# Kernel tuning notes

Measured on AMD Instinct MI355X. Metric: run time of the kernel, lower is better.

Reference implementation:

```python
import jax, jax.numpy as jnp
import numpy as np

N_NODES = 50000
N_EDGES = 100000
N_PAIRS = 1600000
IN_DIM = 2816
MAP_HID = 512
IN_CH = 512
HID_CH = 256
OUT_CH = 128


def _dense(x, W, b):
    return x @ W + b


def setup_inputs() -> dict:
    key = jax.random.key(0)
    ks = jax.random.split(key, 20)
    m_emb = jax.random.normal(ks[0], (N_NODES, IN_DIM), dtype=jnp.float32)
    he_v_idx_pos = jax.random.randint(ks[1], (N_PAIRS,), 0, N_NODES)
    he_e_idx_pos = jnp.sort(jax.random.randint(ks[2], (N_PAIRS,), 0, N_EDGES))
    he_v_idx_neg = jax.random.randint(ks[3], (N_PAIRS,), 0, N_NODES)
    he_e_idx_neg = jnp.sort(jax.random.randint(ks[4], (N_PAIRS,), 0, N_EDGES))

    def lin(k, din, dout):
        k1, k2 = jax.random.split(k)
        s = 1.0 / np.sqrt(din)
        W = jax.random.uniform(k1, (din, dout), minval=-s, maxval=s, dtype=jnp.float32)
        b = jax.random.uniform(k2, (dout,), minval=-s, maxval=s, dtype=jnp.float32)
        return W, b

    W0, b0 = lin(ks[5], IN_DIM, MAP_HID)
    W1, b1 = lin(ks[6], MAP_HID, MAP_HID)
    W2, b2 = lin(ks[7], MAP_HID, IN_CH)
    Wt1, bt1 = lin(ks[8], IN_CH, HID_CH)   # HGNN layer 1 theta
    Wt2, bt2 = lin(ks[9], HID_CH, OUT_CH)  # HGNN layer 2 theta

    return dict(
        m_emb=m_emb,
        he_v_idx_pos=he_v_idx_pos, he_e_idx_pos=he_e_idx_pos,
        he_v_idx_neg=he_v_idx_neg, he_e_idx_neg=he_e_idx_neg,
        W0=W0, b0=b0, W1=W1, b1=b1, W2=W2, b2=b2,
        Wt1=Wt1, bt1=bt1, Wt2=Wt2, bt2=bt2,
    )


def _hg_mean_aggr(X, v_idx, e_idx, n_edges, n_nodes):
    # v2e: mean of member-vertex features per hyperedge
    e_sum = jax.ops.segment_sum(X[v_idx], e_idx, num_segments=n_edges)
    e_cnt = jax.ops.segment_sum(jnp.ones((v_idx.shape[0],), X.dtype), e_idx, num_segments=n_edges)
    Y = e_sum / jnp.maximum(e_cnt, 1.0)[:, None]
    # e2v: mean of incident-hyperedge features per vertex
    v_sum = jax.ops.segment_sum(Y[e_idx], v_idx, num_segments=n_nodes)
    v_cnt = jax.ops.segment_sum(jnp.ones((e_idx.shape[0],), X.dtype), v_idx, num_segments=n_nodes)
    Xo = v_sum / jnp.maximum(v_cnt, 1.0)[:, None]
    return Xo, Y


def _hgnn_layer(X, v_idx, e_idx, W, b, is_last):
    X = _dense(X, W, b)
    Xo, Y = _hg_mean_aggr(X, v_idx, e_idx, N_EDGES, N_NODES)
    if not is_last:
        Xo = jax.nn.relu(Xo)  # dropout = identity in eval
    return Xo, Y


def reference(m_emb, he_v_idx_pos, he_e_idx_pos, he_v_idx_neg, he_e_idx_neg,
              W0, b0, W1, b1, W2, b2, Wt1, bt1, Wt2, bt2):
    h = jax.nn.relu(_dense(m_emb, W0, b0))
    h = jax.nn.relu(_dense(h, W1, b1))
    feat = _dense(h, W2, b2)  # [N, IN_CH]
    # num_dgnn = 0 -> skip directional conv loop
    X1, X2 = feat, feat
    X1, Y_pos = _hgnn_layer(X1, he_v_idx_pos, he_e_idx_pos, Wt1, bt1, False)
    X2, Y_neg = _hgnn_layer(X2, he_v_idx_neg, he_e_idx_neg, Wt1, bt1, False)
    X1, Y_pos = _hgnn_layer(X1, he_v_idx_pos, he_e_idx_pos, Wt2, bt2, True)
    X2, Y_neg = _hgnn_layer(X2, he_v_idx_neg, he_e_idx_neg, Wt2, bt2, True)
    return (X1, X2, Y_pos, Y_neg)
```

## Files before the change

### kernel.cpp

```cpp
#include <hip/hip_runtime.h>

#define NP 1600000
#define NNODES 50000
#define NEDGES 100000

typedef short bf16x8 __attribute__((ext_vector_type(8)));
typedef short short4b __attribute__((ext_vector_type(4)));
typedef float f32x4 __attribute__((ext_vector_type(4)));
typedef unsigned short ushort_t;

static __device__ __forceinline__ ushort_t f2bf_rne(float f) {
    __bf16 b = (__bf16)f;
    return __builtin_bit_cast(ushort_t, b);
}
static __device__ __forceinline__ float bf2f(ushort_t h) {
    union { float f; unsigned int u; } v; v.u = ((unsigned int)h) << 16;
    return v.f;
}
static __device__ __forceinline__ void addbf8(float* a, uint4 u) {
    unsigned int uu[4] = {u.x, u.y, u.z, u.w};
#pragma unroll
    for (int q = 0; q < 4; ++q) {
        union { float f; unsigned int v; } lo, hi;
        lo.v = uu[q] << 16; hi.v = uu[q] & 0xffff0000u;
        a[2 * q]     += lo.f;
        a[2 * q + 1] += hi.f;
    }
}

static __device__ __forceinline__ void gload_lds16(const void* g, void* lds) {
    __builtin_amdgcn_global_load_lds(
        (const __attribute__((address_space(1))) unsigned int*)g,
        (__attribute__((address_space(3))) unsigned int*)lds, 16, 0, 0);
}

template<bool AF32, bool DORELU, int EPI>
__global__ __launch_bounds__(256, 3) void gemm_bf2(
    const float* __restrict__ Af, const ushort_t* __restrict__ Ab,
    const ushort_t* __restrict__ Bth, const ushort_t* __restrict__ Btl,
    const float* __restrict__ bias,
    float* __restrict__ Cf, ushort_t* __restrict__ Cb,
    int M, int N, int K)
{
    __shared__ ushort_t AsH[4][129][8];
    __shared__ ushort_t BsH[4][129][8];
    __shared__ ushort_t BsL[4][129][8];

    const int tid = threadIdx.x;
    const int wid = tid >> 6;
    const int lane = tid & 63;

    const int nwg = gridDim.x * gridDim.y;
    const int wg  = blockIdx.y * gridDim.x + blockIdx.x;
    const int q = nwg >> 3, r = nwg & 7;
    const int xcd = wg & 7, loc = wg >> 3;
    const int swz = (xcd < r) ? (xcd * (q + 1) + loc)
                              : (r * (q + 1) + (xcd - r) * q + loc);
    const int bn0 = (int)(swz % gridDim.x) * 128;
    const int bm0 = (int)(swz / gridDim.x) * 128;

    const int wrow0 = (wid >> 1) * 64;
    const int wcol0 = (wid & 1) * 64;

    f32x4 acc[4][4];
#pragma unroll
    for (int i = 0; i < 4; ++i)
#pragma unroll
        for (int j = 0; j < 4; ++j) acc[i][j] = (f32x4)0.f;

    const int nk = K >> 5;
    const int kgl = lane >> 4;
    const int r16 = lane & 15;

    const int a_kq   = tid & 7;
    const int a_row0 = tid >> 3;
    const float* aBase[4];
    float4 aPre[4];
    if constexpr (AF32) {
#pragma unroll
        for (int cch = 0; cch < 4; ++cch) {
            int row = cch * 32 + a_row0;
            int rr = bm0 + row; if (rr > M - 1) rr = M - 1;
            aBase[cch] = Af + (size_t)rr * K + a_kq * 4;
            aPre[cch] = *(const float4*)(aBase[cch]);
        }
    }

    for (int kt = 0; kt < nk; ++kt) {
        __syncthreads();
#pragma unroll
        for (int h = 0; h < 2; ++h) {
            int c = bn0 + h * 64 + lane;
            const ushort_t* gbh = Bth + (size_t)c * K + kt * 32 + wid * 8;
            const ushort_t* gbl = Btl + (size_t)c * K + kt * 32 + wid * 8;
            gload_lds16(gbh, &BsH[wid][h * 64][0]);
            gload_lds16(gbl, &BsL[wid][h * 64][0]);
        }
        if constexpr (AF32) {
#pragma unroll
            for (int cch = 0; cch < 4; ++cch) {
                int row = cch * 32 + a_row0;
                float4 v = aPre[cch];
                short4b hi;
                hi[0] = (short)f2bf_rne(v.x); hi[1] = (short)f2bf_rne(v.y);
                hi[2] = (short)f2bf_rne(v.z); hi[3] = (short)f2bf_rne(v.w);
                int kg = a_kq >> 1, j0 = (a_kq & 1) * 4;
                *(short4b*)&AsH[kg][row][j0] = hi;
            }
        } else {
#pragma unroll
            for (int h = 0; h < 2; ++h) {
                int rr = bm0 + h * 64 + lane; if (rr > M - 1) rr = M - 1;
                gload_lds16(Ab + (size_t)rr * K + kt * 32 + wid * 8,
                            &AsH[wid][h * 64][0]);
            }
        }
        __syncthreads();

        if constexpr (AF32) {
            if (kt + 1 < nk) {
#pragma unroll
                for (int cch = 0; cch < 4; ++cch)
                    aPre[cch] = *(const float4*)(aBase[cch] + (kt + 1) * 32);
            }
        }

        bf16x8 ah[4], bh[4], bl[4];
#pragma unroll
        for (int mi = 0; mi < 4; ++mi)
            ah[mi] = *(const bf16x8*)&AsH[kgl][wrow0 + mi * 16 + r16][0];
#pragma unroll
        for (int ni = 0; ni < 4; ++ni) {
            bh[ni] = *(const bf16x8*)&BsH[kgl][wcol0 + ni * 16 + r16][0];
            bl[ni] = *(const bf16x8*)&BsL[kgl][wcol0 + ni * 16 + r16][0];
        }
#pragma unroll
        for (int mi = 0; mi < 4; ++mi)
#pragma unroll
            for (int ni = 0; ni < 4; ++ni) {
                acc[mi][ni] = __builtin_amdgcn_mfma_f32_16x16x32_bf16(ah[mi], bh[ni], acc[mi][ni], 0, 0, 0);
                acc[mi][ni] = __builtin_amdgcn_mfma_f32_16x16x32_bf16(ah[mi], bl[ni], acc[mi][ni], 0, 0, 0);
            }
    }

    const int rg4 = (lane >> 4) * 4;
#pragma unroll
    for (int ni = 0; ni < 4; ++ni) {
        int gcol = bn0 + wcol0 + ni * 16 + r16;
        float bb = bias[gcol];
#pragma unroll
        for (int mi = 0; mi < 4; ++mi)
#pragma unroll
            for (int rg = 0; rg < 4; ++rg) {
                int grow = bm0 + wrow0 + mi * 16 + rg4 + rg;
                if (grow < M) {
                    float v = acc[mi][ni][rg] + bb;
                    if constexpr (DORELU) v = fmaxf(v, 0.f);
                    if constexpr (EPI == 0) Cf[(size_t)grow * N + gcol] = v;
                    else                    Cb[(size_t)grow * N + gcol] = f2bf_rne(v);
                }
            }
    }
}

__global__ __launch_bounds__(256) void prep_and_csr(
    const float* __restrict__ W0, const float* __restrict__ W1,
    const float* __restrict__ W2, const float* __restrict__ Wt1,
    const float* __restrict__ Wt2,
    ushort_t* __restrict__ W0tH, ushort_t* __restrict__ W0tL,
    ushort_t* __restrict__ W1tH, ushort_t* __restrict__ W1tL,
    ushort_t* __restrict__ W2tH, ushort_t* __restrict__ W2tL,
    ushort_t* __restrict__ Wt1tH, ushort_t* __restrict__ Wt1tL,
    ushort_t* __restrict__ Wt2tH, ushort_t* __restrict__ Wt2tL,
    const int* __restrict__ ePos, const int* __restrict__ eNeg,
    const int* __restrict__ vPos, const int* __restrict__ vNeg,
    int* __restrict__ e_off, int* __restrict__ v_cnt)
{
    const int bsel = blockIdx.x;
    if (bsel >= 2080) {
        const int rel = bsel - 2080;
        const int sign = rel >> 10;
        const int* e_idx = sign ? eNeg : ePos;
        const int* v_idx = sign ? vNeg : vPos;
        int* o  = e_off + sign * (NEDGES + 1);
        int* vc = v_cnt + sign * NNODES;
        int i = (rel & 1023) * 256 + threadIdx.x;
        const int stride = 1024 * 256;
        for (; i < NP; i += stride) {
            int cur = e_idx[i];
            int prev = (i > 0) ? e_idx[i - 1] : -1;
            for (int e = prev + 1; e <= cur; ++e) o[e] = i;
            if (i == NP - 1)
                for (int e = cur + 1; e <= NEDGES; ++e) o[e] = NP;
            atomicAdd(&vc[v_idx[i]], 1);
        }
        return;
    }
    const float* W; ushort_t* H; ushort_t* L; int K, N, nx, rel;
    if (bsel < 1408)      { W = W0;  H = W0tH;  L = W0tL;  K = 2816; N = 512; nx = 16; rel = bsel; }
    else if (bsel < 1664) { W = W1;  H = W1tH;  L = W1tL;  K = 512;  N = 512; nx = 16; rel = bsel - 1408; }
    else if (bsel < 1920) { W = W2;  H = W2tH;  L = W2tL;  K = 512;  N = 512; nx = 16; rel = bsel - 1664; }
    else if (bsel < 2048) { W = Wt1; H = Wt1tH; L = Wt1tL; K = 512;  N = 256; nx = 8;  rel = bsel - 1920; }
    else                  { W = Wt2; H = Wt2tH; L = Wt2tL; K = 256;  N = 128; nx = 4;  rel = bsel - 2048; }
    const int n0 = (rel % nx) * 32, k0 = (rel / nx) * 32;

    __shared__ float T[32][33];
    const int c = threadIdx.x & 31, r8 = threadIdx.x >> 5;
#pragma unroll
    for (int i = 0; i < 4; ++i)
        T[r8 + i * 8][c] = W[(size_t)(k0 + r8 + i * 8) * N + n0 + c];
    __syncthreads();
#pragma unroll
    for (int i = 0; i < 4; ++i) {
        int nr = r8 + i * 8;
        float v = T[c][nr];
        ushort_t h = f2bf_rne(v);
        H[(size_t)(n0 + nr) * K + k0 + c] = h;
        L[(size_t)(n0 + nr) * K + k0 + c] = f2bf_rne(v - bf2f(h));
    }
}

__global__ __launch_bounds__(1024) void exscan2(const int* __restrict__ cnt,
                                                int* __restrict__ off)
{
    const int sign = blockIdx.x;
    const int* c = cnt + sign * NNODES;
    int* o = off + sign * (NNODES + 1);
    __shared__ int sums[1024];
    const int t = threadIdx.x;
    const int per = (NNODES + 1023) >> 10;
    const int b = t * per;
    const int e = min(b + per, NNODES);
    int s = 0;
    for (int i = b; i < e; ++i) s += c[i];
    sums[t] = s;
    __syncthreads();
    for (int d = 1; d < 1024; d <<= 1) {
        int v = (t >= d) ? sums[t - d] : 0;
        __syncthreads();
        sums[t] += v;
        __syncthreads();
    }
    int run = (t > 0) ? sums[t - 1] : 0;
    for (int i = b; i < e; ++i) { o[i] = run; run += c[i]; }
    if (t == 1023) o[NNODES] = run;
}

__global__ void scatter_both(const int* __restrict__ vPos, const int* __restrict__ vNeg,
                             const int* __restrict__ ePos, const int* __restrict__ eNeg,
                             const int* __restrict__ v_off, int* __restrict__ v_cnt,
                             int* __restrict__ e_by_v)
{
    const int sign = blockIdx.y;
    const int* v_idx = sign ? vNeg : vPos;
    const int* e_idx = sign ? eNeg : ePos;
    const int* vo = v_off + sign * (NNODES + 1);
    int* vc = v_cnt + sign * NNODES;
    int* ebv = e_by_v + sign * NP;
    int i = blockIdx.x * blockDim.x + threadIdx.x;
    int stride = gridDim.x * blockDim.x;
    for (; i < NP; i += stride) {
        int v = v_idx[i];
        int pos = atomicSub(&vc[v], 1) - 1;
        ebv[vo[v] + pos] = e_idx[i];
    }
}

template<bool SRCBF, int C, bool DORELU, int EPI>
__global__ __launch_bounds__(256) void seg_mean2(
    const void* __restrict__ src, long long src_stride,
    const int* __restrict__ idx0, const int* __restrict__ idx1,
    const int* __restrict__ off_base, int off_stride,
    float* __restrict__ dstf, long long dstf_stride,
    ushort_t* __restrict__ dB, long long dB_stride,
    int nseg)
{
    constexpr int ES  = SRCBF ? 2 : 4;
    constexpr int LPR = (C * ES) / 16;
    constexpr int MPI = 64 / LPR;
    constexpr int CPL = 16 / ES;

    const int sign = blockIdx.y;
    const int* idx = sign ? idx1 : idx0;
    const int* off = off_base + (size_t)sign * off_stride;

    const int wave = threadIdx.x >> 6, lane = threadIdx.x & 63;
    const int s = blockIdx.x * 4 + wave;
    if (s >= nseg) return;
    const int b = off[s], e = off[s + 1];
    const int sub = lane / LPR;
    const int cbase = (lane % LPR) * CPL;

    float a0[CPL], a1[CPL], a2[CPL], a3[CPL];
#pragma unroll
    for (int k = 0; k < CPL; ++k) { a0[k] = 0.f; a1[k] = 0.f; a2[k] = 0.f; a3[k] = 0.f; }

    int j = b + sub;
    if constexpr (SRCBF) {
        const ushort_t* sp = (const ushort_t*)src + (size_t)sign * src_stride;
        for (; j + 3 * MPI < e; j += 4 * MPI) {
            int i0 = idx[j], i1 = idx[j + MPI], i2 = idx[j + 2 * MPI], i3 = idx[j + 3 * MPI];
            uint4 u0 = *(const uint4*)(sp + (size_t)i0 * C + cbase);
            uint4 u1 = *(const uint4*)(sp + (size_t)i1 * C + cbase);
            uint4 u2 = *(const uint4*)(sp + (size_t)i2 * C + cbase);
            uint4 u3 = *(const uint4*)(sp + (size_t)i3 * C + cbase);
            addbf8(a0, u0); addbf8(a1, u1); addbf8(a2, u2); addbf8(a3, u3);
        }
        for (; j < e; j += MPI) {
            uint4 u = *(const uint4*)(sp + (size_t)idx[j] * C + cbase);
            addbf8(a0, u);
        }
    } else {
        const float* sp = (const float*)src + (size_t)sign * src_stride;
        for (; j + 3 * MPI < e; j += 4 * MPI) {
            int i0 = idx[j], i1 = idx[j + MPI], i2 = idx[j + 2 * MPI], i3 = idx[j + 3 * MPI];
            float4 v0 = *(const float4*)(sp + (size_t)i0 * C + cbase);
            float4 v1 = *(const float4*)(sp + (size_t)i1 * C + cbase);
            float4 v2 = *(const float4*)(sp + (size_t)i2 * C + cbase);
            float4 v3 = *(const float4*)(sp + (size_t)i3 * C + cbase);
            a0[0] += v0.x; a0[1] += v0.y; a0[2] += v0.z; a0[3] += v0.w;
            a1[0] += v1.x; a1[1] += v1.y; a1[2] += v1.z; a1[3] += v1.w;
            a2[0] += v2.x; a2[1] += v2.y; a2[2] += v2.z; a2[3] += v2.w;
            a3[0] += v3.x; a3[1] += v3.y; a3[2] += v3.z; a3[3] += v3.w;
        }
        for (; j < e; j += MPI) {
            float4 v = *(const float4*)(sp + (size_t)idx[j] * C + cbase);
            a0[0] += v.x; a0[1] += v.y; a0[2] += v.z; a0[3] += v.w;
        }
    }

    float acc[CPL];
#pragma unroll
    for (int k = 0; k < CPL; ++k) acc[k] = (a0[k] + a1[k]) + (a2[k] + a3[k]);

#pragma unroll
    for (int st = LPR; st < 64; st <<= 1)
#pragma unroll
        for (int k = 0; k < CPL; ++k)
            acc[k] += __shfl_xor(acc[k], st);

    if (lane < LPR) {
        const float inv = 1.f / fmaxf((float)(e - b), 1.f);
#pragma unroll
        for (int k = 0; k < CPL; ++k) {
            float v = acc[k] * inv;
            if constexpr (DORELU) v = fmaxf(v, 0.f);
            if constexpr (EPI == 0) {
                (dstf + (size_t)sign * dstf_stride)[(size_t)s * C + cbase + k] = v;
            } else if constexpr (EPI == 1) {
                (dB + (size_t)sign * dB_stride)[(size_t)s * C + cbase + k] = f2bf_rne(v);
            } else {
                (dstf + (size_t)sign * dstf_stride)[(size_t)s * C + cbase + k] = v;
                (dB + (size_t)sign * dB_stride)[(size_t)s * C + cbase + k] = f2bf_rne(v);
            }
        }
    }
}

extern "C" void kernel_launch(void* const* d_in, const int* in_sizes, int n_in,
                              void* d_out, int out_size, void* d_ws, size_t ws_size,
                              hipStream_t stream)
{
    const float* m_emb = (const float*)d_in[0];
    const int*   v_pos = (const int*)d_in[1];
    const int*   e_pos = (const int*)d_in[2];
    const int*   v_neg = (const int*)d_in[3];
    const int*   e_neg = (const int*)d_in[4];
    const float* W0  = (const float*)d_in[5];
    const float* b0  = (const float*)d_in[6];
    const float* W1  = (const float*)d_in[7];
    const float* b1  = (const float*)d_in[8];
    const float* W2  = (const float*)d_in[9];
    const float* b2  = (const float*)d_in[10];
    const float* Wt1 = (const float*)d_in[11];
    const float* bt1 = (const float*)d_in[12];
    const float* Wt2 = (const float*)d_in[13];
    const float* bt2 = (const float*)d_in[14];
    float* out = (float*)d_out;

    char* p = (char*)d_ws;
    auto carve = [&](size_t bytes) { char* r = p; p += (bytes + 255) & ~(size_t)255; return r; };
    const size_t NA = (size_t)NNODES * 512;
    ushort_t* regionA = (ushort_t*)carve(NA * 2);
    ushort_t* regionB = (ushort_t*)carve(NA * 2);
    ushort_t* Y1b  = (ushort_t*)carve((size_t)2 * NEDGES * 256 * 2);
    ushort_t* Xt1b = (ushort_t*)carve((size_t)NNODES * 256 * 2);
    ushort_t* Xt2b = (ushort_t*)carve((size_t)2 * NNODES * 128 * 2);
    ushort_t* Y2b  = (ushort_t*)carve((size_t)2 * NEDGES * 128 * 2);

    ushort_t* h0b = regionA;
    ushort_t* h1b = regionB;
    ushort_t* featb = regionA;
    ushort_t* X1b = regionB;

    ushort_t* W0tH  = (ushort_t*)carve((size_t)512 * 2816 * 2);
    ushort_t* W0tL  = (ushort_t*)carve((size_t)512 * 2816 * 2);
    ushort_t* W1tH  = (ushort_t*)carve((size_t)512 * 512 * 2);
    ushort_t* W1tL  = (ushort_t*)carve((size_t)512 * 512 * 2);
    ushort_t* W2tH  = (ushort_t*)carve((size_t)512 * 512 * 2);
    ushort_t* W2tL  = (ushort_t*)carve((size_t)512 * 512 * 2);
    ushort_t* Wt1tH = (ushort_t*)carve((size_t)256 * 512 * 2);
    ushort_t* Wt1tL = (ushort_t*)carve((size_t)256 * 512 * 2);
    ushort_t* Wt2tH = (ushort_t*)carve((size_t)128 * 256 * 2);
    ushort_t* Wt2tL = (ushort_t*)carve((size_t)128 * 256 * 2);
    int* e_off  = (int*)carve((size_t)2 * (NEDGES + 1) * 4);
    int* v_off  = (int*)carve((size_t)2 * (NNODES + 1) * 4);
    int* e_by_v = (int*)carve((size_t)2 * NP * 4);
    int* v_cnt  = (int*)carve((size_t)2 * NNODES * 4);

    const int MB = (NNODES + 127) / 128;
    const int MB2 = (2 * NNODES + 127) / 128;

    hipMemsetAsync(v_cnt, 0, (size_t)2 * NNODES * 4, stream);
    prep_and_csr<<<2080 + 2048, 256, 0, stream>>>(
        W0, W1, W2, Wt1, Wt2,
        W0tH, W0tL, W1tH, W1tL, W2tH, W2tL, Wt1tH, Wt1tL, Wt2tH, Wt2tL,
        e_pos, e_neg, v_pos, v_neg, e_off, v_cnt);
    exscan2<<<2, 1024, 0, stream>>>(v_cnt, v_off);
    scatter_both<<<dim3(1024, 2), 256, 0, stream>>>(v_pos, v_neg, e_pos, e_neg,
                                                    v_off, v_cnt, e_by_v);

    gemm_bf2<true, true, 1><<<dim3(4, MB), 256, 0, stream>>>(
        m_emb, nullptr, W0tH, W0tL, b0, nullptr, h0b, NNODES, 512, 2816);
    gemm_bf2<false, true, 1><<<dim3(4, MB), 256, 0, stream>>>(
        nullptr, h0b, W1tH, W1tL, b1, nullptr, h1b, NNODES, 512, 512);
    gemm_bf2<false, false, 1><<<dim3(4, MB), 256, 0, stream>>>(
        nullptr, h1b, W2tH, W2tL, b2, nullptr, featb, NNODES, 512, 512);

    gemm_bf2<false, false, 1><<<dim3(2, MB), 256, 0, stream>>>(
        nullptr, featb, Wt1tH, Wt1tL, bt1, nullptr, Xt1b, NNODES, 256, 512);

    seg_mean2<true, 256, false, 1><<<dim3(NEDGES / 4, 2), 256, 0, stream>>>(
        Xt1b, 0, v_pos, v_neg, e_off, NEDGES + 1,
        nullptr, 0, Y1b, (long long)NEDGES * 256, NEDGES);
    seg_mean2<true, 256, true, 1><<<dim3(NNODES / 4, 2), 256, 0, stream>>>(
        Y1b, (long long)NEDGES * 256, e_by_v, e_by_v + NP, v_off, NNODES + 1,
        nullptr, 0, X1b, (long long)NNODES * 256, NNODES);

    gemm_bf2<false, false, 1><<<dim3(1, MB2), 256, 0, stream>>>(
        nullptr, X1b, Wt2tH, Wt2tL, bt2, nullptr, Xt2b, 2 * NNODES, 128, 256);

    seg_mean2<true, 128, false, 3><<<dim3(NEDGES / 4, 2), 256, 0, stream>>>(
        Xt2b, (long long)NNODES * 128, v_pos, v_neg, e_off, NEDGES + 1,
        out + 12800000, 12800000LL, Y2b, (long long)NEDGES * 128, NEDGES);
    seg_mean2<true, 128, false, 0><<<dim3(NNODES / 4, 2), 256, 0, stream>>>(
        Y2b, (long long)NEDGES * 128, e_by_v, e_by_v + NP, v_off, NNODES + 1,
        out, 6400000LL, nullptr, 0, NNODES);
}
```

Baseline: 1.955 ms.

## Pre-convert m_emb to bf16 and deepen GEMM K-tile to 64

The fp32-to-bf16 conversion of m_emb moves out of the first GEMM's inner loop into a separate conversion phase folded into the prep kernel. Every GEMM now loads A through direct global-to-LDS copies with a K tile of 64, which halves the number of barrier pairs per K step. Workspace buffers are overlaid on one large region to hold the converted input. This costs an extra full read and write pass over the large input and doubles LDS use per block, which may reduce occupancy.

```diff
diff --git a/kernel.cpp b/kernel.cpp
--- a/kernel.cpp
+++ b/kernel.cpp
@@ -34,17 +34,17 @@
         (__attribute__((address_space(3))) unsigned int*)lds, 16, 0, 0);
 }
 
-template<bool AF32, bool DORELU, int EPI>
+template<bool DORELU, int EPI>
 __global__ __launch_bounds__(256, 3) void gemm_bf2(
-    const float* __restrict__ Af, const ushort_t* __restrict__ Ab,
+    const ushort_t* __restrict__ Ab,
     const ushort_t* __restrict__ Bth, const ushort_t* __restrict__ Btl,
     const float* __restrict__ bias,
     float* __restrict__ Cf, ushort_t* __restrict__ Cb,
     int M, int N, int K)
 {
-    __shared__ ushort_t AsH[4][129][8];
-    __shared__ ushort_t BsH[4][129][8];
-    __shared__ ushort_t BsL[4][129][8];
+    __shared__ ushort_t As[8][129][8];
+    __shared__ ushort_t BsH[8][129][8];
+    __shared__ ushort_t BsL[8][129][8];
 
     const int tid = threadIdx.x;
     const int wid = tid >> 6;
@@ -68,79 +68,47 @@
 #pragma unroll
         for (int j = 0; j < 4; ++j) acc[i][j] = (f32x4)0.f;
 
-    const int nk = K >> 5;
+    const int nk = K >> 6;
     const int kgl = lane >> 4;
     const int r16 = lane & 15;
 
-    const int a_kq   = tid & 7;
-    const int a_row0 = tid >> 3;
-    const float* aBase[4];
-    float4 aPre[4];
-    if constexpr (AF32) {
-#pragma unroll
-        for (int cch = 0; cch < 4; ++cch) {
-            int row = cch * 32 + a_row0;
-            int rr = bm0 + row; if (rr > M - 1) rr = M - 1;
-            aBase[cch] = Af + (size_t)rr * K + a_kq * 4;
-            aPre[cch] = *(const float4*)(aBase[cch]);
-        }
-    }
-
     for (int kt = 0; kt < nk; ++kt) {
         __syncthreads();
 #pragma unroll
-        for (int h = 0; h < 2; ++h) {
-            int c = bn0 + h * 64 + lane;
-            const ushort_t* gbh = Bth + (size_t)c * K + kt * 32 + wid * 8;
-            const ushort_t* gbl = Btl + (size_t)c * K + kt * 32 + wid * 8;
-            gload_lds16(gbh, &BsH[wid][h * 64][0]);
-            gload_lds16(gbl, &BsL[wid][h * 64][0]);
-        }
-        if constexpr (AF32) {
-#pragma unroll
-            for (int cch = 0; cch < 4; ++cch) {
-                int row = cch * 32 + a_row0;
-                float4 v = aPre[cch];
-                short4b hi;
-                hi[0] = (short)f2bf_rne(v.x); hi[1] = (short)f2bf_rne(v.y);
-                hi[2] = (short)f2bf_rne(v.z); hi[3] = (short)f2bf_rne(v.w);
-                int kg = a_kq >> 1, j0 = (a_kq & 1) * 4;
-                *(short4b*)&AsH[kg][row][j0] = hi;
-            }
-        } else {
+        for (int pp = 0; pp < 2; ++pp) {
+            const int pl = wid + pp * 4;
+            const int kofs = kt * 64 + pl * 8;
 #pragma unroll
             for (int h = 0; h < 2; ++h) {
                 int rr = bm0 + h * 64 + lane; if (rr > M - 1) rr = M - 1;
-                gload_lds16(Ab + (size_t)rr * K + kt * 32 + wid * 8,
-                            &AsH[wid][h * 64][0]);
+                int cc = bn0 + h * 64 + lane;
+                gload_lds16(Ab  + (size_t)rr * K + kofs, &As[pl][h * 64][0]);
+                gload_lds16(Bth + (size_t)cc * K + kofs, &BsH[pl][h * 64][0]);
+                gload_lds16(Btl + (size_t)cc * K + kofs, &BsL[pl][h * 64][0]);
             }
         }
         __syncthreads();
 
-        if constexpr (AF32) {
-            if (kt + 1 < nk) {
-#pragma unroll
-                for (int cch = 0; cch < 4; ++cch)
-                    aPre[cch] = *(const float4*)(aBase[cch] + (kt + 1) * 32);
+#pragma unroll
+        for (int ks = 0; ks < 2; ++ks) {
+            const int kp = ks * 4 + kgl;
+            bf16x8 ah[4], bh[4], bl[4];
+#pragma unroll
+            for (int mi = 0; mi < 4; ++mi)
+                ah[mi] = *(const bf16x8*)&As[kp][wrow0 + mi * 16 + r16][0];
+#pragma unroll
+            for (int ni = 0; ni < 4; ++ni) {
+                bh[ni] = *(const bf16x8*)&BsH[kp][wcol0 + ni * 16 + r16][0];
+                bl[ni] = *(const bf16x8*)&BsL[kp][wcol0 + ni * 16 + r16][0];
             }
-        }
-
-        bf16x8 ah[4], bh[4], bl[4];
-#pragma unroll
-        for (int mi = 0; mi < 4; ++mi)
-            ah[mi] = *(const bf16x8*)&AsH[kgl][wrow0 + mi * 16 + r16][0];
-#pragma unroll
-        for (int ni = 0; ni < 4; ++ni) {
-            bh[ni] = *(const bf16x8*)&BsH[kgl][wcol0 + ni * 16 + r16][0];
-            bl[ni] = *(const bf16x8*)&BsL[kgl][wcol0 + ni * 16 + r16][0];
-        }
-#pragma unroll
-        for (int mi = 0; mi < 4; ++mi)
-#pragma unroll
-            for (int ni = 0; ni < 4; ++ni) {
-                acc[mi][ni] = __builtin_amdgcn_mfma_f32_16x16x32_bf16(ah[mi], bh[ni], acc[mi][ni], 0, 0, 0);
-                acc[mi][ni] = __builtin_amdgcn_mfma_f32_16x16x32_bf16(ah[mi], bl[ni], acc[mi][ni], 0, 0, 0);
-            }
+#pragma unroll
+            for (int mi = 0; mi < 4; ++mi)
+#pragma unroll
+                for (int ni = 0; ni < 4; ++ni) {
+                    acc[mi][ni] = __builtin_amdgcn_mfma_f32_16x16x32_bf16(ah[mi], bh[ni], acc[mi][ni], 0, 0, 0);
+                    acc[mi][ni] = __builtin_amdgcn_mfma_f32_16x16x32_bf16(ah[mi], bl[ni], acc[mi][ni], 0, 0, 0);
+                }
+        }
     }
 
     const int rg4 = (lane >> 4) * 4;
@@ -163,7 +131,7 @@
     }
 }
 
-__global__ __launch_bounds__(256) void prep_and_csr(
+__global__ __launch_bounds__(256) void prep_csr_conv(
     const float* __restrict__ W0, const float* __restrict__ W1,
     const float* __restrict__ W2, const float* __restrict__ Wt1,
     const float* __restrict__ Wt2,
@@ -174,9 +142,28 @@
     ushort_t* __restrict__ Wt2tH, ushort_t* __restrict__ Wt2tL,
     const int* __restrict__ ePos, const int* __restrict__ eNeg,
     const int* __restrict__ vPos, const int* __restrict__ vNeg,
-    int* __restrict__ e_off, int* __restrict__ v_cnt)
+    int* __restrict__ e_off, int* __restrict__ v_cnt,
+    const float* __restrict__ m_emb, ushort_t* __restrict__ m_embB)
 {
     const int bsel = blockIdx.x;
+    if (bsel >= 4128) {
+        const long long n8 = (long long)NNODES * 2816 / 8;
+        long long t = (long long)(bsel - 4128) * 256 + threadIdx.x;
+        const long long stride = 4096LL * 256;
+        for (; t < n8; t += stride) {
+            const float* s = m_emb + t * 8;
+            float4 v0 = *(const float4*)s;
+            float4 v1 = *(const float4*)(s + 4);
+            short4b c0, c1;
+            c0[0] = (short)f2bf_rne(v0.x); c0[1] = (short)f2bf_rne(v0.y);
+            c0[2] = (short)f2bf_rne(v0.z); c0[3] = (short)f2bf_rne(v0.w);
+            c1[0] = (short)f2bf_rne(v1.x); c1[1] = (short)f2bf_rne(v1.y);
+            c1[2] = (short)f2bf_rne(v1.z); c1[3] = (short)f2bf_rne(v1.w);
+            *(short4b*)(m_embB + t * 8)     = c0;
+            *(short4b*)(m_embB + t * 8 + 4) = c1;
+        }
+        return;
+    }
     if (bsel >= 2080) {
         const int rel = bsel - 2080;
         const int sign = rel >> 10;
@@ -382,16 +369,17 @@
     auto carve = [&](size_t bytes) { char* r = p; p += (bytes + 255) & ~(size_t)255; return r; };
     const size_t NA = (size_t)NNODES * 512;
     ushort_t* regionA = (ushort_t*)carve(NA * 2);
-    ushort_t* regionB = (ushort_t*)carve(NA * 2);
-    ushort_t* Y1b  = (ushort_t*)carve((size_t)2 * NEDGES * 256 * 2);
-    ushort_t* Xt1b = (ushort_t*)carve((size_t)NNODES * 256 * 2);
-    ushort_t* Xt2b = (ushort_t*)carve((size_t)2 * NNODES * 128 * 2);
-    ushort_t* Y2b  = (ushort_t*)carve((size_t)2 * NEDGES * 128 * 2);
-
-    ushort_t* h0b = regionA;
-    ushort_t* h1b = regionB;
+    char* U = carve((size_t)NNODES * 2816 * 2);
+
+    ushort_t* m_embB = (ushort_t*)U;
+    ushort_t* h0b   = regionA;
     ushort_t* featb = regionA;
-    ushort_t* X1b = regionB;
+    ushort_t* h1b   = (ushort_t*)U;
+    ushort_t* X1b   = (ushort_t*)U;
+    ushort_t* Y1b   = (ushort_t*)(U + (size_t)52 * 1024 * 1024);
+    ushort_t* Xt1b  = (ushort_t*)(U + (size_t)156 * 1024 * 1024);
+    ushort_t* Xt2b  = (ushort_t*)(U + (size_t)182 * 1024 * 1024);
+    ushort_t* Y2b   = (ushort_t*)(U + (size_t)208 * 1024 * 1024);
 
     ushort_t* W0tH  = (ushort_t*)carve((size_t)512 * 2816 * 2);
     ushort_t* W0tL  = (ushort_t*)carve((size_t)512 * 2816 * 2);
@@ -412,23 +400,24 @@
     const int MB2 = (2 * NNODES + 127) / 128;
 
     hipMemsetAsync(v_cnt, 0, (size_t)2 * NNODES * 4, stream);
-    prep_and_csr<<<2080 + 2048, 256, 0, stream>>>(
+    prep_csr_conv<<<8224, 256, 0, stream>>>(
         W0, W1, W2, Wt1, Wt2,
         W0tH, W0tL, W1tH, W1tL, W2tH, W2tL, Wt1tH, Wt1tL, Wt2tH, Wt2tL,
-        e_pos, e_neg, v_pos, v_neg, e_off, v_cnt);
+        e_pos, e_neg, v_pos, v_neg, e_off, v_cnt,
+        m_emb, m_embB);
     exscan2<<<2, 1024, 0, stream>>>(v_cnt, v_off);
     scatter_both<<<dim3(1024, 2), 256, 0, stream>>>(v_pos, v_neg, e_pos, e_neg,
                                                     v_off, v_cnt, e_by_v);
 
-    gemm_bf2<true, true, 1><<<dim3(4, MB), 256, 0, stream>>>(
-        m_emb, nullptr, W0tH, W0tL, b0, nullptr, h0b, NNODES, 512, 2816);
-    gemm_bf2<false, true, 1><<<dim3(4, MB), 256, 0, stream>>>(
-        nullptr, h0b, W1tH, W1tL, b1, nullptr, h1b, NNODES, 512, 512);
-    gemm_bf2<false, false, 1><<<dim3(4, MB), 256, 0, stream>>>(
-        nullptr, h1b, W2tH, W2tL, b2, nullptr, featb, NNODES, 512, 512);
-
-    gemm_bf2<false, false, 1><<<dim3(2, MB), 256, 0, stream>>>(
-        nullptr, featb, Wt1tH, Wt1tL, bt1, nullptr, Xt1b, NNODES, 256, 512);
+    gemm_bf2<true, 1><<<dim3(4, MB), 256, 0, stream>>>(
+        m_embB, W0tH, W0tL, b0, nullptr, h0b, NNODES, 512, 2816);
+    gemm_bf2<true, 1><<<dim3(4, MB), 256, 0, stream>>>(
+        h0b, W1tH, W1tL, b1, nullptr, h1b, NNODES, 512, 512);
+    gemm_bf2<false, 1><<<dim3(4, MB), 256, 0, stream>>>(
+        h1b, W2tH, W2tL, b2, nullptr, featb, NNODES, 512, 512);
+
+    gemm_bf2<false, 1><<<dim3(2, MB), 256, 0, stream>>>(
+        featb, Wt1tH, Wt1tL, bt1, nullptr, Xt1b, NNODES, 256, 512);
 
     seg_mean2<true, 256, false, 1><<<dim3(NEDGES / 4, 2), 256, 0, stream>>>(
         Xt1b, 0, v_pos, v_neg, e_off, NEDGES + 1,
@@ -437,8 +426,8 @@
         Y1b, (long long)NEDGES * 256, e_by_v, e_by_v + NP, v_off, NNODES + 1,
         nullptr, 0, X1b, (long long)NNODES * 256, NNODES);
 
-    gemm_bf2<false, false, 1><<<dim3(1, MB2), 256, 0, stream>>>(
-        nullptr, X1b, Wt2tH, Wt2tL, bt2, nullptr, Xt2b, 2 * NNODES, 128, 256);
+    gemm_bf2<false, 1><<<dim3(1, MB2), 256, 0, stream>>>(
+        X1b, Wt2tH, Wt2tL, bt2, nullptr, Xt2b, 2 * NNODES, 128, 256);
 
     seg_mean2<true, 128, false, 3><<<dim3(NEDGES / 4, 2), 256, 0, stream>>>(
         Xt2b, (long long)NNODES * 128, v_pos, v_neg, e_off, NEDGES + 1,
```

Result: slower. 2.164 ms (+10.7%).
